# Kernel tuning notes

Hardware: AMD Instinct MI355X
Metric: run time of the kernel (lower is better)

Reference implementation:

```python
import jax, jax.numpy as jnp
import numpy as np

B, N, T = 2, 207, 864
L = 12           # patch_size
D = 96           # embed_dim
EPS = 1e-8
TAU = 1.0


def setup_inputs() -> dict:
    key = jax.random.key(0)
    k1, k2, k3, k4, k5 = jax.random.split(key, 5)
    return {
        "long_term_history": jax.random.normal(k1, (B, N, 1, T), dtype=jnp.float32),
        "adj_mx": jax.random.uniform(k2, (N, N), dtype=jnp.float32),
        "uniform_noise": jax.random.uniform(k3, (N, N), dtype=jnp.float32),
        "conv_weight": jax.random.normal(k4, (D, N, L), dtype=jnp.float32) * 0.02,
        "conv_bias": jax.random.normal(k5, (D,), dtype=jnp.float32) * 0.02,
        "k": 10,
    }


def _sample_k_neighbor_soft(adj_mx, uniform_noise, k):
    n = adj_mx.shape[0]
    logits = jnp.log(jax.nn.relu(adj_mx) + EPS)
    gumbel = -jnp.log(-jnp.log(uniform_noise + EPS))
    soft = jax.nn.softmax((logits + gumbel) / TAU, axis=1)          # [N, N]
    _, topk_idx = jax.lax.top_k(soft, k)                             # [N, k]
    hard = jnp.zeros_like(soft).at[jnp.arange(n)[:, None], topk_idx].set(1.0)
    return soft * hard                                               # [N, N]


def reference(long_term_history, adj_mx, uniform_noise, conv_weight, conv_bias, k):
    b, n, _, t = long_term_history.shape
    p = t // L
    mask = _sample_k_neighbor_soft(adj_mx, uniform_noise, k)         # [N, N]
    # expanded_history[b,i,j,t] = x[b,i,0,t]; neighbors = mask[i,j] * x[b,i,0,t]
    x = long_term_history[:, :, 0, :]                                # [B, N, T]
    neighbors = mask[None, :, :, None] * x[:, :, None, :]            # [B, N, N, T] (dense blow-up, as in source)
    xp = neighbors.reshape(b, n, n, p, L)                            # split T -> P patches of length L
    # Conv2d(N -> D, kernel (L,1), stride (L,1)) == contraction over (neighbor channel j, in-patch l)
    out = jnp.einsum('bijpl,djl->bidp', xp, conv_weight) + conv_bias[None, None, :, None]
    return out                                                       # [B, N, D, P]
```

## Files before the change

kernel.cpp:

```cpp
#include <hip/hip_runtime.h>
#include <math.h>

#define NN 207
#define BB 2
#define TT 864
#define LL 12
#define DD 96
#define PP 72
#define EPSF 1e-8f

__global__ __launch_bounds__(256) void weff_kernel(
    const float* __restrict__ adj,
    const float* __restrict__ noise,
    const float* __restrict__ W,
    const int*   __restrict__ kptr,
    float*       __restrict__ weff)
{
    __shared__ float s_score[NN];
    __shared__ float s_topS[32];
    __shared__ int   s_topI[32];

    const int i   = blockIdx.x;
    const int tid = threadIdx.x;
    const int kk  = min(*kptr, 32);

    if (tid < NN) {
        float a = fmaxf(adj[i * NN + tid], 0.0f) + EPSF;
        float u = noise[i * NN + tid] + EPSF;
        s_score[tid] = logf(a) - logf(-logf(u));
    }
    __syncthreads();

    if (tid < 64) {
        const int lane = tid;
        float v[4], orig[4];
        #pragma unroll
        for (int q = 0; q < 4; ++q) {
            int c = lane + 64 * q;
            v[q] = (c < NN) ? s_score[c] : -INFINITY;
            orig[q] = v[q];
        }
        float m = 0.0f, myv = 0.0f; int myi = 0;
        for (int it = 0; it < kk; ++it) {
            float bv = v[0]; int bi = lane;
            #pragma unroll
            for (int q = 1; q < 4; ++q)
                if (v[q] > bv) { bv = v[q]; bi = lane + 64 * q; }
            #pragma unroll
            for (int off = 32; off > 0; off >>= 1) {
                float ov = __shfl_xor(bv, off);
                int   oi = __shfl_xor(bi, off);
                if (ov > bv || (ov == bv && oi < bi)) { bv = ov; bi = oi; }
            }
            if (it == 0) m = bv;
            if (lane == it) { myv = bv; myi = bi; }
            if ((bi & 63) == lane) v[bi >> 6] = -INFINITY;
        }
        float se = 0.0f;
        #pragma unroll
        for (int q = 0; q < 4; ++q) {
            int c = lane + 64 * q;
            if (c < NN) se += expf(orig[q] - m);
        }
        #pragma unroll
        for (int off = 32; off > 0; off >>= 1) se += __shfl_xor(se, off);
        if (lane < kk) {
            s_topS[lane] = expf(myv - m) / se;
            s_topI[lane] = myi;
        }
    }
    __syncthreads();

    {
        const float4* W4  = (const float4*)W;
        float4*       wf4 = (float4*)weff + i * (DD * 3);
        for (int e = tid; e < DD * 3; e += 256) {
            int d = e / 3, c = e - d * 3;
            float4 acc = {0.f, 0.f, 0.f, 0.f};
            for (int t = 0; t < kk; ++t) {
                float s  = s_topS[t];
                float4 w = W4[(d * NN + s_topI[t]) * 3 + c];
                acc.x += s * w.x; acc.y += s * w.y;
                acc.z += s * w.z; acc.w += s * w.w;
            }
            wf4[e] = acc;
        }
    }
}

__global__ __launch_bounds__(256) void out_kernel(
    const float* __restrict__ x,
    const float* __restrict__ weff,
    const float* __restrict__ bias,
    float*       __restrict__ out)
{
    const unsigned TOTAL = BB * NN * DD * (PP / 4);
    unsigned e = blockIdx.x * 256u + threadIdx.x;
    if (e >= TOTAL) return;

    unsigned c  = e % 18u;
    unsigned r  = e / 18u;
    unsigned d  = r % (unsigned)DD;
    unsigned bi = r / (unsigned)DD;
    unsigned i  = bi % (unsigned)NN;

    const float4* x4 = (const float4*)x + (size_t)bi * (TT / 4) + c * 12u;
    const float4* w4 = (const float4*)weff + ((size_t)i * DD + d) * 3u;

    float4 w0 = w4[0], w1 = w4[1], w2 = w4[2];
    float  bd = bias[d];

    float o[4];
    #pragma unroll
    for (int q = 0; q < 4; ++q) {
        float4 a0 = x4[q * 3 + 0];
        float4 a1 = x4[q * 3 + 1];
        float4 a2 = x4[q * 3 + 2];
        float s = bd;
        s += a0.x * w0.x; s += a0.y * w0.y; s += a0.z * w0.z; s += a0.w * w0.w;
        s += a1.x * w1.x; s += a1.y * w1.y; s += a1.z * w1.z; s += a1.w * w1.w;
        s += a2.x * w2.x; s += a2.y * w2.y; s += a2.z * w2.z; s += a2.w * w2.w;
        o[q] = s;
    }
    float4 val = {o[0], o[1], o[2], o[3]};
    ((float4*)out)[e] = val;
}

extern "C" void kernel_launch(void* const* d_in, const int* in_sizes, int n_in,
                              void* d_out, int out_size, void* d_ws, size_t ws_size,
                              hipStream_t stream) {
    const float* x     = (const float*)d_in[0];
    const float* adj   = (const float*)d_in[1];
    const float* noise = (const float*)d_in[2];
    const float* W     = (const float*)d_in[3];
    const float* bias  = (const float*)d_in[4];
    const int*   kptr  = (const int*)d_in[5];
    float* out  = (float*)d_out;
    float* weff = (float*)d_ws;

    weff_kernel<<<NN, 256, 0, stream>>>(adj, noise, W, kptr, weff);

    const int total4 = BB * NN * DD * (PP / 4);
    out_kernel<<<(total4 + 255) / 256, 256, 0, stream>>>(x, weff, bias, out);
}
```

Before: 87.68 us.

## Fuse neighbor-weight computation and patch projection into one kernel

Merges the per-node effective-weight kernel and the output projection kernel into a single kernel with one block per node. The effective weights are kept in shared memory instead of being written to and re-read from a global workspace, and one launch is removed. In exchange the output phase runs on only 207 blocks, which reduces parallelism and latency hiding for the memory-bound store phase.

```diff
diff --git a/kernel.cpp b/kernel.cpp
--- a/kernel.cpp
+++ b/kernel.cpp
@@ -9,14 +9,17 @@
 #define PP 72
 #define EPSF 1e-8f
 
-__global__ __launch_bounds__(256) void weff_kernel(
+__global__ __launch_bounds__(512) void stpe_fused_kernel(
+    const float* __restrict__ x,
     const float* __restrict__ adj,
     const float* __restrict__ noise,
     const float* __restrict__ W,
+    const float* __restrict__ bias,
     const int*   __restrict__ kptr,
-    float*       __restrict__ weff)
+    float*       __restrict__ out)
 {
     __shared__ float s_score[NN];
+    __shared__ float s_weff[DD * LL];
     __shared__ float s_topS[32];
     __shared__ int   s_topI[32];
 
@@ -72,9 +75,9 @@
     __syncthreads();
 
     {
-        const float4* W4  = (const float4*)W;
-        float4*       wf4 = (float4*)weff + i * (DD * 3);
-        for (int e = tid; e < DD * 3; e += 256) {
+        const float4* W4 = (const float4*)W;
+        float4* weff4 = (float4*)s_weff;
+        for (int e = tid; e < DD * 3; e += 512) {
             int d = e / 3, c = e - d * 3;
             float4 acc = {0.f, 0.f, 0.f, 0.f};
             for (int t = 0; t < kk; ++t) {
@@ -83,47 +86,39 @@
                 acc.x += s * w.x; acc.y += s * w.y;
                 acc.z += s * w.z; acc.w += s * w.w;
             }
-            wf4[e] = acc;
+            weff4[e] = acc;
         }
     }
-}
+    __syncthreads();
 
-__global__ __launch_bounds__(256) void out_kernel(
-    const float* __restrict__ x,
-    const float* __restrict__ weff,
-    const float* __restrict__ bias,
-    float*       __restrict__ out)
-{
-    const unsigned TOTAL = BB * NN * DD * (PP / 4);
-    unsigned e = blockIdx.x * 256u + threadIdx.x;
-    if (e >= TOTAL) return;
-
-    unsigned c  = e % 18u;
-    unsigned r  = e / 18u;
-    unsigned d  = r % (unsigned)DD;
-    unsigned bi = r / (unsigned)DD;
-    unsigned i  = bi % (unsigned)NN;
-
-    const float4* x4 = (const float4*)x + (size_t)bi * (TT / 4) + c * 12u;
-    const float4* w4 = (const float4*)weff + ((size_t)i * DD + d) * 3u;
-
-    float4 w0 = w4[0], w1 = w4[1], w2 = w4[2];
-    float  bd = bias[d];
-
-    float o[4];
-    #pragma unroll
-    for (int q = 0; q < 4; ++q) {
-        float4 a0 = x4[q * 3 + 0];
-        float4 a1 = x4[q * 3 + 1];
-        float4 a2 = x4[q * 3 + 2];
-        float s = bd;
-        s += a0.x * w0.x; s += a0.y * w0.y; s += a0.z * w0.z; s += a0.w * w0.w;
-        s += a1.x * w1.x; s += a1.y * w1.y; s += a1.z * w1.z; s += a1.w * w1.w;
-        s += a2.x * w2.x; s += a2.y * w2.y; s += a2.z * w2.z; s += a2.w * w2.w;
-        o[q] = s;
+    {
+        const float4* xbase = (const float4*)x;
+        float4*       out4  = (float4*)out;
+        for (int e = tid; e < BB * DD * (PP / 4); e += 512) {
+            int b = e / (DD * (PP / 4));
+            int r = e - b * (DD * (PP / 4));
+            int d = r / (PP / 4);
+            int c = r - d * (PP / 4);
+            const float4* x4 = xbase + (size_t)(b * NN + i) * (TT / 4) + c * 12;
+            const float4* w4 = (const float4*)&s_weff[d * LL];
+            float4 w0 = w4[0], w1 = w4[1], w2 = w4[2];
+            float  bd = bias[d];
+            float o[4];
+            #pragma unroll
+            for (int q = 0; q < 4; ++q) {
+                float4 a0 = x4[q * 3 + 0];
+                float4 a1 = x4[q * 3 + 1];
+                float4 a2 = x4[q * 3 + 2];
+                float s = bd;
+                s += a0.x * w0.x; s += a0.y * w0.y; s += a0.z * w0.z; s += a0.w * w0.w;
+                s += a1.x * w1.x; s += a1.y * w1.y; s += a1.z * w1.z; s += a1.w * w1.w;
+                s += a2.x * w2.x; s += a2.y * w2.y; s += a2.z * w2.z; s += a2.w * w2.w;
+                o[q] = s;
+            }
+            float4 val = {o[0], o[1], o[2], o[3]};
+            out4[((size_t)(b * NN + i) * DD + d) * (PP / 4) + c] = val;
+        }
     }
-    float4 val = {o[0], o[1], o[2], o[3]};
-    ((float4*)out)[e] = val;
 }
 
 extern "C" void kernel_launch(void* const* d_in, const int* in_sizes, int n_in,
@@ -135,11 +130,7 @@
     const float* W     = (const float*)d_in[3];
     const float* bias  = (const float*)d_in[4];
     const int*   kptr  = (const int*)d_in[5];
-    float* out  = (float*)d_out;
-    float* weff = (float*)d_ws;
+    float* out = (float*)d_out;
 
-    weff_kernel<<<NN, 256, 0, stream>>>(adj, noise, W, kptr, weff);
-
-    const int total4 = BB * NN * DD * (PP / 4);
-    out_kernel<<<(total4 + 255) / 256, 256, 0, stream>>>(x, weff, bias, out);
+    stpe_fused_kernel<<<NN, 512, 0, stream>>>(x, adj, noise, W, bias, kptr, out);
 }
```

Result: no change. 87.19 us (-0.6%).
